# Performance work log

Hardware: AMD Instinct MI355X
Metric: run time of the kernel (lower is better)

## Reference

```python
import jax, jax.numpy as jnp
import numpy as np

N_HEADS = 8

def setup_inputs() -> dict:
    key = jax.random.key(0)
    ks = jax.random.split(key, 5)
    C = 256
    x = jax.random.normal(ks[0], (4, C, 48, 48), dtype=jnp.float32)
    w_qkv = jax.random.normal(ks[1], (3 * C, C), dtype=jnp.float32) * (C ** -0.5)
    b_qkv = jax.random.normal(ks[2], (3 * C,), dtype=jnp.float32) * 0.02
    w_proj = jax.random.normal(ks[3], (C, C), dtype=jnp.float32) * (C ** -0.5)
    b_proj = jax.random.normal(ks[4], (C,), dtype=jnp.float32) * 0.02
    return {"x": x, "w_qkv": w_qkv, "b_qkv": b_qkv, "w_proj": w_proj, "b_proj": b_proj}


def reference(x, w_qkv, b_qkv, w_proj, b_proj):
    B, C, H, W = x.shape
    h = N_HEADS
    dh = C // h
    N = H * W
    # flatten spatial dims to tokens: [B, N, C]
    xf = x.reshape(B, C, N).transpose(0, 2, 1)
    # fused qkv projection (torch Linear: y = x @ W.T + b)
    qkv = xf @ w_qkv.T + b_qkv                      # [B, N, 3C]
    qkv = qkv.reshape(B, N, 3, h, dh).transpose(2, 0, 3, 1, 4)  # [3, B, h, N, dh]
    q, k, v = qkv[0], qkv[1], qkv[2]
    scale = dh ** -0.5
    attn = jax.nn.softmax(jnp.einsum('bhnd,bhmd->bhnm', q, k) * scale, axis=-1)
    out = jnp.einsum('bhnm,bhmd->bhnd', attn, v)    # [B, h, N, dh]
    out = out.transpose(0, 2, 1, 3).reshape(B, N, C)
    out = out @ w_proj.T + b_proj                   # [B, N, C]
    return out.transpose(0, 2, 1).reshape(B, C, H, W)
```

## Files before the change

### kernel.cpp

```cpp
#include <hip/hip_runtime.h>
#include <hip/hip_bf16.h>

#define B_    4
#define C_    256
#define NTOK  2304
#define NH    8
#define DH    32

typedef short bf16x8 __attribute__((ext_vector_type(8)));
typedef short bf16x4 __attribute__((ext_vector_type(4)));
typedef float f32x4  __attribute__((ext_vector_type(4)));

__device__ __forceinline__ short rne_bf16(float f) {
    union { float f; unsigned u; } v; v.f = f;
    const unsigned r = v.u + 0x7fffu + ((v.u >> 16) & 1u);
    return (short)(r >> 16);
}
__device__ __forceinline__ unsigned pack2_bf16(float a, float b) {
    return (unsigned)(unsigned short)rne_bf16(a) | ((unsigned)(unsigned short)rne_bf16(b) << 16);
}
__device__ __forceinline__ float fast_exp2(float x) {
#if __has_builtin(__builtin_amdgcn_exp2f)
    return __builtin_amdgcn_exp2f(x);
#else
    return exp2f(x);
#endif
}

__global__ __launch_bounds__(256) void prep_kernel(
    const float* __restrict__ x, const float* __restrict__ wq,
    const float* __restrict__ wp,
    short* __restrict__ xt, short* __restrict__ wqb, short* __restrict__ wpb)
{
    const int blk = blockIdx.x;
    const int t   = threadIdx.x;
    if (blk < 576) {
        const int b  = blk / 144;
        const int rem = blk % 144;
        const int n0 = (rem / 4) * 64;
        const int c0 = (rem % 4) * 64;
        __shared__ float tile[64][65];
        const float* xb = x + ((size_t)b * C_ + c0) * NTOK + n0;
        const int n = t & 63, cc = t >> 6;
        #pragma unroll
        for (int r = 0; r < 16; ++r)
            tile[cc + r * 4][n] = xb[(size_t)(cc + r * 4) * NTOK + n];
        __syncthreads();
        const int nr = t >> 2, cb = (t & 3) * 16;
        short* dst = xt + ((size_t)b * NTOK + n0 + nr) * C_ + c0 + cb;
        bf16x8 v0, v1;
        #pragma unroll
        for (int u = 0; u < 8; ++u) v0[u] = rne_bf16(tile[cb + u][nr]);
        #pragma unroll
        for (int u = 0; u < 8; ++u) v1[u] = rne_bf16(tile[cb + 8 + u][nr]);
        *(bf16x8*)dst = v0;
        *(bf16x8*)(dst + 8) = v1;
    } else {
        const int id = (blk - 576) * 256 + t;
        const int base = id * 16;
        #pragma unroll
        for (int u = 0; u < 4; ++u) {
            const int off = base + u * 4;
            float4 v; short* d;
            if (off < 196608) { v = *(const float4*)(wq + off); d = wqb + off; }
            else { v = *(const float4*)(wp + (off - 196608)); d = wpb + (off - 196608); }
            d[0] = rne_bf16(v.x); d[1] = rne_bf16(v.y);
            d[2] = rne_bf16(v.z); d[3] = rne_bf16(v.w);
        }
    }
}

__global__ __launch_bounds__(256) void qkv_mfma(
    const short* __restrict__ xt,
    const short* __restrict__ wqb,
    const float* __restrict__ bias,
    short* __restrict__ qb, short* __restrict__ kb, short* __restrict__ vt)
{
    __shared__ short Es[4][2560];
    const int wave = threadIdx.x >> 6;
    const int lane = threadIdx.x & 63;
    const int quad = lane >> 4, l16 = lane & 15;
    const int wid  = blockIdx.x * 4 + wave;
    const int b    = wid / 864;
    const int rem  = wid % 864;
    const int mt = rem / 12, nt = rem % 12;
    const int m0 = mt * 32, j0 = nt * 64;

    const short* abase = xt + ((size_t)b * NTOK + m0 + l16) * C_ + quad * 8;
    const short* bbase = wqb + (size_t)(j0 + l16) * C_ + quad * 8;

    f32x4 acc[2][4] = {};
    for (int k0 = 0; k0 < C_; k0 += 32) {
        bf16x8 af[2], bfr[4];
        #pragma unroll
        for (int i = 0; i < 2; ++i)
            af[i] = *(const bf16x8*)(abase + (size_t)i * 16 * C_ + k0);
        #pragma unroll
        for (int j = 0; j < 4; ++j)
            bfr[j] = *(const bf16x8*)(bbase + (size_t)j * 16 * C_ + k0);
        #pragma unroll
        for (int i = 0; i < 2; ++i)
            #pragma unroll
            for (int j = 0; j < 4; ++j)
                acc[i][j] = __builtin_amdgcn_mfma_f32_16x16x32_bf16(af[i], bfr[j], acc[i][j], 0, 0, 0);
    }

    short* Ew = Es[wave];
    const int three = j0 >> 8;
    if (three < 2) {
        const float sc = (three == 0) ? 0.25503486f : 1.0f;
        #pragma unroll
        for (int j = 0; j < 4; ++j) {
            const float bv = bias[j0 + j * 16 + l16];
            #pragma unroll
            for (int i = 0; i < 2; ++i)
                #pragma unroll
                for (int r = 0; r < 4; ++r) {
                    const int n_l = i * 16 + quad * 4 + r;
                    Ew[n_l * 72 + j * 16 + l16] = rne_bf16((acc[i][j][r] + bv) * sc);
                }
        }
        const int n_l = lane & 31, hh = lane >> 5;
        const int head = ((j0 + hh * 32) >> 5) & 7;
        short* dst = ((three == 0) ? qb : kb)
                   + ((size_t)(b * NH + head) * NTOK + m0 + n_l) * DH;
        #pragma unroll
        for (int s = 0; s < 4; ++s)
            *(bf16x8*)(dst + s * 8) = *(const bf16x8*)&Ew[n_l * 72 + hh * 32 + s * 8];
    } else {
        #pragma unroll
        for (int j = 0; j < 4; ++j) {
            const float bv = bias[j0 + j * 16 + l16];
            const int j_l = j * 16 + l16;
            #pragma unroll
            for (int i = 0; i < 2; ++i) {
                const int nb = i * 16 + quad * 4;
                *(unsigned*)&Ew[j_l * 40 + nb] =
                    pack2_bf16(acc[i][j][0] + bv, acc[i][j][1] + bv);
                *(unsigned*)&Ew[j_l * 40 + nb + 2] =
                    pack2_bf16(acc[i][j][2] + bv, acc[i][j][3] + bv);
            }
        }
        #pragma unroll
        for (int p = 0; p < 4; ++p) {
            const int j_r = p * 16 + (lane >> 2);
            const int seg = (lane & 3) * 8;
            const int head = ((j0 + j_r) >> 5) & 7;
            const int d    = j_r & 31;
            *(bf16x8*)(vt + ((size_t)(b * NH + head) * DH + d) * NTOK + m0 + seg) =
                *(const bf16x8*)&Ew[j_r * 40 + seg];
        }
    }
}

__global__ __launch_bounds__(256) void attn_kernel(
    const short* __restrict__ qg,
    const short* __restrict__ kg,
    const short* __restrict__ vg,
    float* __restrict__ po,
    float* __restrict__ pl)
{
    const int bh   = blockIdx.y;
    const int q0   = blockIdx.x * 64;
    const int half = blockIdx.z;
    const int t    = threadIdx.x;
    const int wave = t >> 6;
    const int lane = t & 63;
    const int quad = lane >> 4;
    const int l16  = lane & 15;

    __shared__ short Ks[64][40];
    __shared__ short Vt[32][72];
    __shared__ short Ps[4][16][68];

    const short* kbase = kg + (size_t)bh * NTOK * DH;
    const short* vbase = vg + (size_t)bh * DH * NTOK;

    const short* qptr = qg + ((size_t)bh * NTOK + q0 + wave * 16 + l16) * DH + quad * 8;
    const bf16x8 qf = *(const bf16x8*)qptr;

    f32x4 Oc0 = {0.f, 0.f, 0.f, 0.f};
    f32x4 Oc1 = {0.f, 0.f, 0.f, 0.f};
    float lpart[4] = {0.f, 0.f, 0.f, 0.f};

    const int kbeg = half * (NTOK / 2);
    const int kend = kbeg + (NTOK / 2);
    for (int kt = kbeg; kt < kend; kt += 64) {
        {
            const int kr = t >> 2, ksg = t & 3;
            *(bf16x8*)&Ks[kr][ksg * 8] =
                *(const bf16x8*)(kbase + (size_t)(kt + kr) * DH + ksg * 8);
            const int vr = t >> 3, vsg = t & 7;
            *(bf16x8*)&Vt[vr][vsg * 8] =
                *(const bf16x8*)(vbase + (size_t)vr * NTOK + kt + vsg * 8);
        }
        __syncthreads();

        f32x4 S[4];
        #pragma unroll
        for (int jt = 0; jt < 4; ++jt) {
            const bf16x8 kf = *(const bf16x8*)&Ks[jt * 16 + l16][quad * 8];
            f32x4 z = {0.f, 0.f, 0.f, 0.f};
            S[jt] = __builtin_amdgcn_mfma_f32_16x16x32_bf16(qf, kf, z, 0, 0, 0);
        }

        #pragma unroll
        for (int jt = 0; jt < 4; ++jt) {
            #pragma unroll
            for (int r = 0; r < 4; ++r) {
                const float p = fast_exp2(S[jt][r]);
                lpart[r] += p;
                Ps[wave][quad * 4 + r][jt * 16 + l16] = rne_bf16(p);
            }
        }

        #pragma unroll
        for (int jc = 0; jc < 2; ++jc) {
            const bf16x4 p0 = *(const bf16x4*)&Ps[wave][l16][jc * 32 + quad * 8];
            const bf16x4 p1 = *(const bf16x4*)&Ps[wave][l16][jc * 32 + quad * 8 + 4];
            bf16x8 af;
            af[0] = p0[0]; af[1] = p0[1]; af[2] = p0[2]; af[3] = p0[3];
            af[4] = p1[0]; af[5] = p1[1]; af[6] = p1[2]; af[7] = p1[3];
            const bf16x8 b0 = *(const bf16x8*)&Vt[l16][jc * 32 + quad * 8];
            const bf16x8 b1 = *(const bf16x8*)&Vt[16 + l16][jc * 32 + quad * 8];
            Oc0 = __builtin_amdgcn_mfma_f32_16x16x32_bf16(af, b0, Oc0, 0, 0, 0);
            Oc1 = __builtin_amdgcn_mfma_f32_16x16x32_bf16(af, b1, Oc1, 0, 0, 0);
        }
        __syncthreads();
    }

    #pragma unroll
    for (int off = 1; off < 16; off <<= 1) {
        #pragma unroll
        for (int r = 0; r < 4; ++r)
            lpart[r] += __shfl_xor(lpart[r], off, 64);
    }

    const size_t rowbase = ((size_t)half * 32 + bh) * NTOK + q0 + wave * 16 + quad * 4;
    float* obase = po + rowbase * DH + l16;
    #pragma unroll
    for (int r = 0; r < 4; ++r) {
        obase[(size_t)r * DH]      = Oc0[r];
        obase[(size_t)r * DH + 16] = Oc1[r];
    }
    if (l16 == 0) {
        float* lb = pl + rowbase;
        #pragma unroll
        for (int r = 0; r < 4; ++r) lb[r] = lpart[r];
    }
}

__global__ __launch_bounds__(256) void combine_kernel(
    const float* __restrict__ po, const float* __restrict__ pl,
    short* __restrict__ ob)
{
    const int gid = blockIdx.x * 256 + threadIdx.x;
    const int row = gid >> 2;
    const int seg = (gid & 3) * 8;
    const float inv = 1.f / (pl[row] + pl[73728 + row]);
    const float* p0 = po + (size_t)row * DH + seg;
    const float* p1 = po + (size_t)73728 * DH + (size_t)row * DH + seg;
    f32x4 a0 = *(const f32x4*)p0;
    f32x4 a1 = *(const f32x4*)(p0 + 4);
    f32x4 b0 = *(const f32x4*)p1;
    f32x4 b1 = *(const f32x4*)(p1 + 4);
    bf16x8 o;
    #pragma unroll
    for (int u = 0; u < 4; ++u) o[u]     = rne_bf16((a0[u] + b0[u]) * inv);
    #pragma unroll
    for (int u = 0; u < 4; ++u) o[4 + u] = rne_bf16((a1[u] + b1[u]) * inv);
    *(bf16x8*)(ob + (size_t)row * DH + seg) = o;
}

__global__ __launch_bounds__(256) void proj_mfma(
    const short* __restrict__ ab,
    const short* __restrict__ wpb,
    const float* __restrict__ bias,
    float* __restrict__ out)
{
    __shared__ float Ep[4][2304];
    const int wave = threadIdx.x >> 6;
    const int lane = threadIdx.x & 63;
    const int quad = lane >> 4, l16 = lane & 15;
    const int wid  = blockIdx.x * 4 + wave;
    const int b    = wid / 288;
    const int rem  = wid % 288;
    const int mt = rem / 4, ct = rem % 4;
    const int m0 = mt * 32, c0 = ct * 64;

    const short* bbase = wpb + (size_t)(c0 + l16) * C_ + quad * 8;

    f32x4 acc[2][4] = {};
    for (int kt = 0; kt < 8; ++kt) {
        const short* abase = ab + ((size_t)(b * NH + kt) * NTOK + m0 + l16) * DH + quad * 8;
        bf16x8 af[2], bfr[4];
        #pragma unroll
        for (int i = 0; i < 2; ++i)
            af[i] = *(const bf16x8*)(abase + (size_t)i * 16 * DH);
        #pragma unroll
        for (int j = 0; j < 4; ++j)
            bfr[j] = *(const bf16x8*)(bbase + (size_t)j * 16 * C_ + kt * 32);
        #pragma unroll
        for (int i = 0; i < 2; ++i)
            #pragma unroll
            for (int j = 0; j < 4; ++j)
                acc[i][j] = __builtin_amdgcn_mfma_f32_16x16x32_bf16(af[i], bfr[j], acc[i][j], 0, 0, 0);
    }

    float* Ew = Ep[wave];
    #pragma unroll
    for (int j = 0; j < 4; ++j) {
        const int j_l = j * 16 + l16;
        const float bv = bias[c0 + j_l];
        #pragma unroll
        for (int i = 0; i < 2; ++i) {
            f32x4 st = {acc[i][j][0] + bv, acc[i][j][1] + bv,
                        acc[i][j][2] + bv, acc[i][j][3] + bv};
            *(f32x4*)&Ew[j_l * 36 + i * 16 + quad * 4] = st;
        }
    }
    #pragma unroll
    for (int p = 0; p < 8; ++p) {
        const int c_r = p * 8 + (lane >> 3);
        const int seg = (lane & 7) * 4;
        *(float4*)(out + ((size_t)b * C_ + c0 + c_r) * NTOK + m0 + seg) =
            *(const float4*)&Ew[c_r * 36 + seg];
    }
}

extern "C" void kernel_launch(void* const* d_in, const int* in_sizes, int n_in,
                              void* d_out, int out_size, void* d_ws, size_t ws_size,
                              hipStream_t stream) {
    const float* x      = (const float*)d_in[0];
    const float* w_qkv  = (const float*)d_in[1];
    const float* b_qkv  = (const float*)d_in[2];
    const float* w_proj = (const float*)d_in[3];
    const float* b_proj = (const float*)d_in[4];
    float* out = (float*)d_out;

    const size_t SZ = (size_t)B_ * NH * NTOK * DH;
    short* xt  = (short*)d_ws;
    short* wqb = xt + SZ;
    short* wpb = wqb + 196608;
    short* qb  = wpb + 65536;
    short* kb  = qb + SZ;
    short* vt  = kb + SZ;
    short* abf = vt + SZ;
    float* po  = (float*)(abf + SZ);
    float* pl  = po + 2 * SZ;

    prep_kernel<<<640, 256, 0, stream>>>(x, w_qkv, w_proj, xt, wqb, wpb);
    qkv_mfma<<<864, 256, 0, stream>>>(xt, wqb, b_qkv, qb, kb, vt);
    attn_kernel<<<dim3(36, 32, 2), 256, 0, stream>>>(qb, kb, vt, po, pl);
    combine_kernel<<<1152, 256, 0, stream>>>(po, pl, abf);
    proj_mfma<<<288, 256, 0, stream>>>(abf, wpb, b_proj, out);
}
```

Baseline: 173.4 us.

## Fuse split-K combine into projection GEMM and register-prefetch K/V tiles

Removes the separate combine kernel: the projection GEMM now reads both fp32 partial attention outputs and their row sums, normalizes them and converts to bf16 on the fly as it builds its A fragments. This drops one launch and the bf16 intermediate write and read. Separately, the attention loop now prefetches the next K/V tile into registers while it computes on the current shared-memory tile, so global load latency overlaps with MFMA work. The cost is that the projection kernel reads fp32 data, twice the bytes of the old bf16 input, and repeats the normalization across column tiles. The prefetch also adds register pressure.

```diff
diff --git a/kernel.cpp b/kernel.cpp
--- a/kernel.cpp
+++ b/kernel.cpp
@@ -185,16 +185,21 @@
 
     const int kbeg = half * (NTOK / 2);
     const int kend = kbeg + (NTOK / 2);
+
+    const int kr = t >> 2, ksg = t & 3;
+    const int vr = t >> 3, vsg = t & 7;
+
+    bf16x8 kreg = *(const bf16x8*)(kbase + (size_t)(kbeg + kr) * DH + ksg * 8);
+    bf16x8 vreg = *(const bf16x8*)(vbase + (size_t)vr * NTOK + kbeg + vsg * 8);
+
     for (int kt = kbeg; kt < kend; kt += 64) {
-        {
-            const int kr = t >> 2, ksg = t & 3;
-            *(bf16x8*)&Ks[kr][ksg * 8] =
-                *(const bf16x8*)(kbase + (size_t)(kt + kr) * DH + ksg * 8);
-            const int vr = t >> 3, vsg = t & 7;
-            *(bf16x8*)&Vt[vr][vsg * 8] =
-                *(const bf16x8*)(vbase + (size_t)vr * NTOK + kt + vsg * 8);
-        }
+        *(bf16x8*)&Ks[kr][ksg * 8] = kreg;
+        *(bf16x8*)&Vt[vr][vsg * 8] = vreg;
         __syncthreads();
+
+        const int ktn = (kt + 64 < kend) ? kt + 64 : kbeg;
+        kreg = *(const bf16x8*)(kbase + (size_t)(ktn + kr) * DH + ksg * 8);
+        vreg = *(const bf16x8*)(vbase + (size_t)vr * NTOK + ktn + vsg * 8);
 
         f32x4 S[4];
         #pragma unroll
@@ -250,30 +255,9 @@
     }
 }
 
-__global__ __launch_bounds__(256) void combine_kernel(
-    const float* __restrict__ po, const float* __restrict__ pl,
-    short* __restrict__ ob)
-{
-    const int gid = blockIdx.x * 256 + threadIdx.x;
-    const int row = gid >> 2;
-    const int seg = (gid & 3) * 8;
-    const float inv = 1.f / (pl[row] + pl[73728 + row]);
-    const float* p0 = po + (size_t)row * DH + seg;
-    const float* p1 = po + (size_t)73728 * DH + (size_t)row * DH + seg;
-    f32x4 a0 = *(const f32x4*)p0;
-    f32x4 a1 = *(const f32x4*)(p0 + 4);
-    f32x4 b0 = *(const f32x4*)p1;
-    f32x4 b1 = *(const f32x4*)(p1 + 4);
-    bf16x8 o;
-    #pragma unroll
-    for (int u = 0; u < 4; ++u) o[u]     = rne_bf16((a0[u] + b0[u]) * inv);
-    #pragma unroll
-    for (int u = 0; u < 4; ++u) o[4 + u] = rne_bf16((a1[u] + b1[u]) * inv);
-    *(bf16x8*)(ob + (size_t)row * DH + seg) = o;
-}
-
 __global__ __launch_bounds__(256) void proj_mfma(
-    const short* __restrict__ ab,
+    const float* __restrict__ po,
+    const float* __restrict__ pl,
     const short* __restrict__ wpb,
     const float* __restrict__ bias,
     float* __restrict__ out)
@@ -289,14 +273,27 @@
     const int m0 = mt * 32, c0 = ct * 64;
 
     const short* bbase = wpb + (size_t)(c0 + l16) * C_ + quad * 8;
+    const size_t PO_OFF = (size_t)32 * NTOK * DH;
+    const size_t PL_OFF = (size_t)32 * NTOK;
 
     f32x4 acc[2][4] = {};
     for (int kt = 0; kt < 8; ++kt) {
-        const short* abase = ab + ((size_t)(b * NH + kt) * NTOK + m0 + l16) * DH + quad * 8;
         bf16x8 af[2], bfr[4];
         #pragma unroll
-        for (int i = 0; i < 2; ++i)
-            af[i] = *(const bf16x8*)(abase + (size_t)i * 16 * DH);
+        for (int i = 0; i < 2; ++i) {
+            const size_t row = (size_t)(b * NH + kt) * NTOK + m0 + i * 16 + l16;
+            const float inv = 1.f / (pl[row] + pl[PL_OFF + row]);
+            const float* p0 = po + row * DH + quad * 8;
+            const f32x4 a0 = *(const f32x4*)p0;
+            const f32x4 a1 = *(const f32x4*)(p0 + 4);
+            const f32x4 b0 = *(const f32x4*)(p0 + PO_OFF);
+            const f32x4 b1 = *(const f32x4*)(p0 + PO_OFF + 4);
+            #pragma unroll
+            for (int u = 0; u < 4; ++u) {
+                af[i][u]     = rne_bf16((a0[u] + b0[u]) * inv);
+                af[i][4 + u] = rne_bf16((a1[u] + b1[u]) * inv);
+            }
+        }
         #pragma unroll
         for (int j = 0; j < 4; ++j)
             bfr[j] = *(const bf16x8*)(bbase + (size_t)j * 16 * C_ + kt * 32);
@@ -345,13 +342,11 @@
     short* qb  = wpb + 65536;
     short* kb  = qb + SZ;
     short* vt  = kb + SZ;
-    short* abf = vt + SZ;
-    float* po  = (float*)(abf + SZ);
+    float* po  = (float*)(vt + SZ);
     float* pl  = po + 2 * SZ;
 
     prep_kernel<<<640, 256, 0, stream>>>(x, w_qkv, w_proj, xt, wqb, wpb);
     qkv_mfma<<<864, 256, 0, stream>>>(xt, wqb, b_qkv, qb, kb, vt);
     attn_kernel<<<dim3(36, 32, 2), 256, 0, stream>>>(qb, kb, vt, po, pl);
-    combine_kernel<<<1152, 256, 0, stream>>>(po, pl, abf);
-    proj_mfma<<<288, 256, 0, stream>>>(abf, wpb, b_proj, out);
-}
+    proj_mfma<<<288, 256, 0, stream>>>(po, pl, wpb, b_proj, out);
+}
```

Measured after the change: 173.6 us. About the same (+0.1%).
